# Kernel optimization log

Measured on AMD Instinct MI355X. Metric: run time of the kernel, lower is better.

Reference implementation:

```python
import jax, jax.numpy as jnp
import numpy as np

B, LAT, CIN, W, K, F = 16, 512, 512, 4096, 3, 512

def setup_inputs() -> dict:
    key = jax.random.key(0)
    k1, k2, k3, k4 = jax.random.split(key, 4)
    latent = jax.random.normal(k1, (B, LAT), jnp.float32)
    content = jax.random.normal(k2, (B, CIN, W), jnp.float32)
    # glorot_uniform for affine weight
    lim = np.sqrt(6.0 / (LAT + CIN))
    affine_w = jax.random.uniform(k3, (LAT, CIN), jnp.float32, -lim, lim)
    affine_b = jnp.zeros((1, CIN), jnp.float32)
    # he_normal for conv kernel (fan_in = K*CIN)
    kernel_w = jax.random.normal(k4, (K, CIN, F), jnp.float32) * np.sqrt(2.0 / (K * CIN))
    kernel_b = jnp.zeros((1, F, 1), jnp.float32)
    return {"latent": latent, "content": content, "affine_w": affine_w,
            "affine_b": affine_b, "kernel_w": kernel_w, "kernel_b": kernel_b}

def reference(latent, content, affine_w, affine_b, kernel_w, kernel_b):
    # style affine: [B, CIN]
    affine = latent @ affine_w + affine_b
    # demod scale per (b, f): 1/sqrt(sum_{k,c} (kernel[k,c,f]*affine[b,c])^2 + 1e-8)
    demod = jax.lax.rsqrt(jnp.einsum('kcf,bc->bf', kernel_w * kernel_w,
                                     affine * affine) + 1e-8)
    # modulate input instead of per-sample weights (mathematically identical,
    # avoids batch-as-groups grouped conv): x[b,c,w] = content * affine[b,c]
    x = content * affine[:, :, None]
    # shared-kernel conv1d, NCW / SAME; filter layout [K, CIN, F] == HIO
    y = jax.lax.conv_general_dilated(
        x, kernel_w, window_strides=(1,), padding='SAME',
        dimension_numbers=('NCH', 'HIO', 'NCH'))
    y = y * demod[:, :, None] + kernel_b  # [B, F, W]
    return jnp.where(y >= 0, y, 0.2 * y)  # leaky_relu(0.2)
```

## Files before the change

### kernel.cpp

```cpp
#include <hip/hip_runtime.h>
#include <hip/hip_bf16.h>

#define Bn   16
#define LATn 512
#define Cn   512
#define Wn   4096
#define Fn   512

using bf16x8 = __attribute__((ext_vector_type(8))) short;
using f32x4  = __attribute__((ext_vector_type(4))) float;

__device__ __forceinline__ unsigned short f2bf(float x) {
    union { float f; unsigned int u; } v; v.f = x;
    unsigned int r = v.u + 0x7fffu + ((v.u >> 16) & 1u);
    return (unsigned short)(r >> 16);
}

__device__ __forceinline__ void gload_lds16(const void* g, void* l) {
    __builtin_amdgcn_global_load_lds(
        (const __attribute__((address_space(1))) unsigned int*)g,
        (__attribute__((address_space(3))) unsigned int*)l, 16, 0, 0);
}

__global__ void k_affine(const float* __restrict__ latent,
                         const float* __restrict__ aw,
                         const float* __restrict__ ab,
                         float* __restrict__ affine,
                         float* __restrict__ zbuf) {
    if (blockIdx.x == 0 && blockIdx.y == 0 && threadIdx.x < 16)
        zbuf[threadIdx.x] = 0.f;
    __shared__ float red[4][64];
    const int t  = threadIdx.x;
    const int cl = t & 63, lq = t >> 6;
    const int c  = blockIdx.x * 64 + cl;
    const int b  = blockIdx.y;
    float s = 0.f;
    #pragma unroll 4
    for (int l = lq * 128; l < lq * 128 + 128; ++l)
        s = fmaf(latent[b * LATn + l], aw[(size_t)l * Cn + c], s);
    red[lq][cl] = s;
    __syncthreads();
    if (t < 64)
        affine[b * Cn + blockIdx.x * 64 + t] =
            red[0][t] + red[1][t] + red[2][t] + red[3][t] + ab[blockIdx.x * 64 + t];
}

__global__ void k_qsum(const float* __restrict__ kw, float* __restrict__ Q) {
    const int i = (blockIdx.x * 256 + threadIdx.x) * 4;
    const float4 a = *(const float4*)&kw[i];
    const float4 b = *(const float4*)&kw[Cn * Fn + i];
    const float4 c = *(const float4*)&kw[2 * Cn * Fn + i];
    float4 q;
    q.x = a.x * a.x + b.x * b.x + c.x * c.x;
    q.y = a.y * a.y + b.y * b.y + c.y * c.y;
    q.z = a.z * a.z + b.z * b.z + c.z * c.z;
    q.w = a.w * a.w + b.w * b.w + c.w * c.w;
    *(float4*)&Q[i] = q;
}

__global__ void k_demod2(const float* __restrict__ Q,
                         const float* __restrict__ affine,
                         float* __restrict__ demod) {
    __shared__ float red[4][64];
    const int t  = threadIdx.x;
    const int fl = t & 63, cq = t >> 6;
    const int f  = blockIdx.x * 64 + fl;
    const int b  = blockIdx.y;
    float s = 0.f;
    #pragma unroll 4
    for (int c = cq * 128; c < cq * 128 + 128; ++c) {
        const float a = affine[b * Cn + c];
        s = fmaf(a * a, Q[(size_t)c * Fn + f], s);
    }
    red[cq][fl] = s;
    __syncthreads();
    if (t < 64)
        demod[b * Fn + blockIdx.x * 64 + t] =
            rsqrtf(red[0][t] + red[1][t] + red[2][t] + red[3][t] + 1e-8f);
}

__global__ void k_tk(const float* __restrict__ kw, unsigned short* __restrict__ kt) {
    __shared__ float lds[32][65];
    const int t  = threadIdx.x;
    const int k  = blockIdx.z;
    const int c0 = blockIdx.x * 32;
    const int f0 = blockIdx.y * 64;
    #pragma unroll
    for (int i = 0; i < 8; ++i) {
        int e = t + 256 * i; int c = e >> 6; int f = e & 63;
        lds[c][f] = kw[((size_t)(k * Cn + c0 + c)) * Fn + f0 + f];
    }
    __syncthreads();
    #pragma unroll
    for (int i = 0; i < 8; ++i) {
        int e = t + 256 * i; int f = e >> 5; int c = e & 31;
        kt[((size_t)(k * Fn + f0 + f)) * Cn + c0 + c] = f2bf(lds[c][f]);
    }
}

__global__ void k_tx(const float* __restrict__ content,
                     const float* __restrict__ affine,
                     unsigned short* __restrict__ xt) {
    __shared__ unsigned short lds[64][72];
    const int t  = threadIdx.x;
    const int b  = blockIdx.z;
    const int c0 = blockIdx.y * 64;
    const int w0 = blockIdx.x * 64;
    #pragma unroll
    for (int i = 0; i < 4; ++i) {
        int e = t + 256 * i;
        int c = e >> 4;
        int w4 = (e & 15) * 4;
        float4 v = *(const float4*)&content[((size_t)(b * Cn + c0 + c)) * Wn + w0 + w4];
        float a = affine[b * Cn + c0 + c];
        int wx = w4 ^ ((c >> 3) << 3);
        unsigned short p[4] = {f2bf(v.x * a), f2bf(v.y * a), f2bf(v.z * a), f2bf(v.w * a)};
        *(uint2*)&lds[c][wx] = *(const uint2*)p;
    }
    __syncthreads();
    #pragma unroll
    for (int i = 0; i < 2; ++i) {
        int e = t + 256 * i;
        int w  = e >> 3;
        int q  = e & 7;
        int c8 = q * 8;
        int wx = w ^ (q << 3);
        unsigned short tmp[8];
        #pragma unroll
        for (int j = 0; j < 8; ++j) tmp[j] = lds[c8 + j][wx];
        *(uint4*)&xt[((size_t)b * Wn + w0 + w) * Cn + c0 + c8] = *(uint4*)tmp;
    }
}

#define BM 256
#define BN 256
#define BK 32
#define KBYTES (3 * BM * BK * 2)
#define BUFB   (KBYTES + BN * BK * 2)
#define SMEMB  (2 * BUFB + 2 * Cn * 2)

extern __shared__ __align__(16) char smem[];

#define ISSUE_XT(dst, c0s) { \
    _Pragma("unroll") for (int i_ = 0; i_ < 2; ++i_) { \
        const int Q_ = i_ * 512 + t; \
        const int r_ = Q_ >> 2; \
        const int j_ = (Q_ & 3) ^ ((r_ >> 1) & 3); \
        gload_lds16(&xt[((size_t)b * Wn + w0 + r_) * Cn + (c0s) + j_ * 8], \
                    (dst) + KBYTES + (size_t)Q_ * 16); } }

#define ISSUE_PLANE(dst, c0s, P) { \
    _Pragma("unroll") for (int i_ = 0; i_ < 2; ++i_) { \
        const int Q_ = i_ * 512 + t; \
        const int r_ = Q_ >> 2; \
        const int j_ = (Q_ & 3) ^ ((r_ >> 1) & 3); \
        gload_lds16(&kt[((size_t)((P) * Fn + f0 + r_)) * Cn + (c0s) + j_ * 8], \
                    (dst) + (size_t)((P) * 1024 + Q_) * 16); } }

#define PHASE(K, VM, ...) { \
    asm volatile("s_waitcnt vmcnt(" #VM ")" ::: "memory"); \
    asm volatile("s_barrier" ::: "memory"); \
    bf16x8 af[8]; bf16x8 bv[4]; \
    _Pragma("unroll") for (int m_ = 0; m_ < 8; ++m_) { \
        const int r_ = wm * 128 + m_ * 16 + l15; \
        af[m_] = *(const bf16x8*)(ka + ((K) * 256 + r_) * 32 + (lhi ^ ((r_ >> 1) & 3)) * 8); } \
    _Pragma("unroll") for (int n_ = 0; n_ < 4; ++n_) { \
        const int rl_ = wn * 64 + n_ * 16 + l15 + (K) - 1; \
        const unsigned short* bp_ = xa + rl_ * 32 + (lhi ^ ((rl_ >> 1) & 3)) * 8; \
        if ((K) == 0 && n_ == 0 && rl_ < 0)   bp_ = halo + c0 + lhi * 8; \
        if ((K) == 2 && n_ == 3 && rl_ > 255) bp_ = halo + 512 + c0 + lhi * 8; \
        bv[n_] = *(const bf16x8*)bp_; } \
    __VA_ARGS__; \
    asm volatile("s_waitcnt lgkmcnt(0)" ::: "memory"); \
    __builtin_amdgcn_sched_barrier(0); \
    __builtin_amdgcn_s_setprio(1); \
    _Pragma("unroll") for (int n_ = 0; n_ < 4; ++n_) \
        _Pragma("unroll") for (int m_ = 0; m_ < 8; ++m_) \
            acc[m_][n_] = __builtin_amdgcn_mfma_f32_16x16x32_bf16(af[m_], bv[n_], acc[m_][n_], 0, 0, 0); \
    __builtin_amdgcn_s_setprio(0); }

__global__ __launch_bounds__(512, 1)
void k_conv(const unsigned short* __restrict__ kt,
            const unsigned short* __restrict__ xt,
            const float* __restrict__ demod,
            const float* __restrict__ kb,
            const float* __restrict__ zbuf,
            float* __restrict__ y) {
    const int t  = threadIdx.x;
    const int w0 = blockIdx.x * BN;
    const int f0 = blockIdx.y * BM;
    const int b  = blockIdx.z;

    const int wave = t >> 6;
    const int lane = t & 63;
    const int wm   = wave >> 2;
    const int wn   = wave & 3;
    const int l15  = lane & 15;
    const int lhi  = lane >> 4;

    unsigned short* halo = (unsigned short*)(smem + 2 * BUFB);

    f32x4 acc[8][4];
    #pragma unroll
    for (int m = 0; m < 8; ++m)
        #pragma unroll
        for (int n = 0; n < 4; ++n)
            #pragma unroll
            for (int r = 0; r < 4; ++r)
                acc[m][n][r] = 0.f;

    if (t < 128) {
        const int h  = t >> 6;
        const int wg = h ? (w0 + BN) : (w0 - 1);
        const unsigned short* src = ((unsigned)wg < (unsigned)Wn)
            ? &xt[((size_t)b * Wn + wg) * Cn + (t & 63) * 8]
            : (const unsigned short*)zbuf;
        gload_lds16(src, halo + (size_t)t * 8);
    }
    ISSUE_XT(smem, 0);
    ISSUE_PLANE(smem, 0, 0);
    ISSUE_PLANE(smem, 0, 1);
    ISSUE_PLANE(smem, 0, 2);

    int cur = 0;
    for (int cc = 0; cc < Cn / BK; ++cc) {
        const unsigned short* ka = (const unsigned short*)(smem + cur * BUFB);
        const unsigned short* xa = ka + 3 * BM * BK;
        char* nbuf = smem + (cur ^ 1) * BUFB;
        const int c0 = cc * BK;
        const int c1 = c0 + BK;
        const bool pf = cc < Cn / BK - 1;
        PHASE(0, 4, if (pf) { ISSUE_XT(nbuf, c1); ISSUE_PLANE(nbuf, c1, 0); });
        PHASE(1, 6, if (pf) { ISSUE_PLANE(nbuf, c1, 1); });
        PHASE(2, 6, if (pf) { ISSUE_PLANE(nbuf, c1, 2); });
        cur ^= 1;
    }

    #pragma unroll
    for (int m = 0; m < 8; ++m) {
        const int fb = f0 + wm * 128 + m * 16 + lhi * 4;
        const float4 dmv = *(const float4*)&demod[b * Fn + fb];
        const float4 kbv = *(const float4*)&kb[fb];
        const float dmf[4] = {dmv.x, dmv.y, dmv.z, dmv.w};
        const float kbf[4] = {kbv.x, kbv.y, kbv.z, kbv.w};
        #pragma unroll
        for (int n = 0; n < 4; ++n) {
            const int w = w0 + wn * 64 + n * 16 + l15;
            #pragma unroll
            for (int r = 0; r < 4; ++r) {
                float v = fmaf(acc[m][n][r], dmf[r], kbf[r]);
                v = (v >= 0.f) ? v : 0.2f * v;
                y[((size_t)(b * Fn + fb + r)) * Wn + w] = v;
            }
        }
    }
}

extern "C" void kernel_launch(void* const* d_in, const int* in_sizes, int n_in,
                              void* d_out, int out_size, void* d_ws, size_t ws_size,
                              hipStream_t stream) {
    const float* latent  = (const float*)d_in[0];
    const float* content = (const float*)d_in[1];
    const float* aw      = (const float*)d_in[2];
    const float* ab      = (const float*)d_in[3];
    const float* kw      = (const float*)d_in[4];
    const float* kb      = (const float*)d_in[5];
    float* y = (float*)d_out;

    char* ws = (char*)d_ws;
    float*          affine = (float*)(ws);
    float*          demod  = (float*)(ws + 32768);
    float*          zbuf   = (float*)(ws + 65536);
    float*          Q      = (float*)(ws + 131072);
    unsigned short* kt     = (unsigned short*)(ws + 131072);
    unsigned short* xt     = (unsigned short*)(ws + 2u * 1024u * 1024u);
    if (ws_size < 2u * 1024u * 1024u + (size_t)Bn * Wn * Cn * 2u) return;

    hipFuncSetAttribute((const void*)k_conv,
                        hipFuncAttributeMaxDynamicSharedMemorySize, SMEMB);

    k_affine<<<dim3(Cn / 64, Bn),           256, 0, stream>>>(latent, aw, ab, affine, zbuf);
    k_qsum  <<<dim3(Cn * Fn / 1024),        256, 0, stream>>>(kw, Q);
    k_demod2<<<dim3(Fn / 64, Bn),           256, 0, stream>>>(Q, affine, demod);
    k_tk    <<<dim3(Cn / 32, Fn / 64, 3),   256, 0, stream>>>(kw, kt);
    k_tx    <<<dim3(Wn / 64, Cn / 64, Bn),  256, 0, stream>>>(content, affine, xt);
    k_conv  <<<dim3(Wn / BN, Fn / BM, Bn),  512, SMEMB, stream>>>(kt, xt, demod, kb, zbuf, y);
}
```

Before: 167.1 us.

## Split conv phases into half-M sub-phases with ping-pong barriers

Each K-plane phase is split into two halves over the M tiles, so each wave loads only 4 A fragments at a time and reuses the B fragments across both halves. The next-chunk prefetch is spread across the sub-phases. Synchronisation changes from per-phase vmcnt waits to a full vmcnt(0) wait at the end of each chunk, with a barrier before and after every MFMA block. This aims to lower register pressure and interleave LDS reads with MFMA work, but it adds barriers and makes the global-load wait coarser.

```diff
diff --git a/kernel.cpp b/kernel.cpp
--- a/kernel.cpp
+++ b/kernel.cpp
@@ -157,27 +157,31 @@
         gload_lds16(&kt[((size_t)((P) * Fn + f0 + r_)) * Cn + (c0s) + j_ * 8], \
                     (dst) + (size_t)((P) * 1024 + Q_) * 16); } }
 
-#define PHASE(K, VM, ...) { \
-    asm volatile("s_waitcnt vmcnt(" #VM ")" ::: "memory"); \
+#define PHASE(K, H, PRE, POSTW) { \
+    if ((H) == 0) { \
+        _Pragma("unroll") for (int n_ = 0; n_ < 4; ++n_) { \
+            const int rl_ = wn * 64 + n_ * 16 + l15 + (K) - 1; \
+            const unsigned short* bp_ = xa + rl_ * 32 + (lhi ^ ((rl_ >> 1) & 3)) * 8; \
+            if ((K) == 0 && n_ == 0 && rl_ < 0)   bp_ = halo + c0 + lhi * 8; \
+            if ((K) == 2 && n_ == 3 && rl_ > 255) bp_ = halo + 512 + c0 + lhi * 8; \
+            bv[n_] = *(const bf16x8*)bp_; } \
+    } \
+    bf16x8 af[4]; \
+    _Pragma("unroll") for (int m_ = 0; m_ < 4; ++m_) { \
+        const int r_ = wm * 128 + ((H) * 4 + m_) * 16 + l15; \
+        af[m_] = *(const bf16x8*)(ka + ((K) * 256 + r_) * 32 + (lhi ^ ((r_ >> 1) & 3)) * 8); } \
+    PRE; \
     asm volatile("s_barrier" ::: "memory"); \
-    bf16x8 af[8]; bf16x8 bv[4]; \
-    _Pragma("unroll") for (int m_ = 0; m_ < 8; ++m_) { \
-        const int r_ = wm * 128 + m_ * 16 + l15; \
-        af[m_] = *(const bf16x8*)(ka + ((K) * 256 + r_) * 32 + (lhi ^ ((r_ >> 1) & 3)) * 8); } \
-    _Pragma("unroll") for (int n_ = 0; n_ < 4; ++n_) { \
-        const int rl_ = wn * 64 + n_ * 16 + l15 + (K) - 1; \
-        const unsigned short* bp_ = xa + rl_ * 32 + (lhi ^ ((rl_ >> 1) & 3)) * 8; \
-        if ((K) == 0 && n_ == 0 && rl_ < 0)   bp_ = halo + c0 + lhi * 8; \
-        if ((K) == 2 && n_ == 3 && rl_ > 255) bp_ = halo + 512 + c0 + lhi * 8; \
-        bv[n_] = *(const bf16x8*)bp_; } \
-    __VA_ARGS__; \
     asm volatile("s_waitcnt lgkmcnt(0)" ::: "memory"); \
     __builtin_amdgcn_sched_barrier(0); \
     __builtin_amdgcn_s_setprio(1); \
     _Pragma("unroll") for (int n_ = 0; n_ < 4; ++n_) \
-        _Pragma("unroll") for (int m_ = 0; m_ < 8; ++m_) \
-            acc[m_][n_] = __builtin_amdgcn_mfma_f32_16x16x32_bf16(af[m_], bv[n_], acc[m_][n_], 0, 0, 0); \
-    __builtin_amdgcn_s_setprio(0); }
+        _Pragma("unroll") for (int m_ = 0; m_ < 4; ++m_) \
+            acc[(H) * 4 + m_][n_] = __builtin_amdgcn_mfma_f32_16x16x32_bf16( \
+                af[m_], bv[n_], acc[(H) * 4 + m_][n_], 0, 0, 0); \
+    __builtin_amdgcn_s_setprio(0); \
+    POSTW; \
+    asm volatile("s_barrier" ::: "memory"); }
 
 __global__ __launch_bounds__(512, 1)
 void k_conv(const unsigned short* __restrict__ kt,
@@ -221,6 +225,8 @@
     ISSUE_PLANE(smem, 0, 0);
     ISSUE_PLANE(smem, 0, 1);
     ISSUE_PLANE(smem, 0, 2);
+    asm volatile("s_waitcnt vmcnt(0)" ::: "memory");
+    asm volatile("s_barrier" ::: "memory");
 
     int cur = 0;
     for (int cc = 0; cc < Cn / BK; ++cc) {
@@ -230,9 +236,13 @@
         const int c0 = cc * BK;
         const int c1 = c0 + BK;
         const bool pf = cc < Cn / BK - 1;
-        PHASE(0, 4, if (pf) { ISSUE_XT(nbuf, c1); ISSUE_PLANE(nbuf, c1, 0); });
-        PHASE(1, 6, if (pf) { ISSUE_PLANE(nbuf, c1, 1); });
-        PHASE(2, 6, if (pf) { ISSUE_PLANE(nbuf, c1, 2); });
+        bf16x8 bv[4];
+        PHASE(0, 0, if (pf) { ISSUE_XT(nbuf, c1); },      )
+        PHASE(0, 1, if (pf) { ISSUE_PLANE(nbuf, c1, 0); },)
+        PHASE(1, 0, if (pf) { ISSUE_PLANE(nbuf, c1, 1); },)
+        PHASE(1, 1, if (pf) { ISSUE_PLANE(nbuf, c1, 2); },)
+        PHASE(2, 0, ,                                     )
+        PHASE(2, 1, , asm volatile("s_waitcnt vmcnt(0)" ::: "memory"))
         cur ^= 1;
     }
 
```

Result: slower. 170.5 us (+2.1%).

## Switch conv GEMM to 32x32 MFMA, merge prep kernels, load halo rows directly

Applied to the files above, without the earlier changes.

The conv main loop now uses 32x32x16 bf16 MFMA tiles in place of 16x16x32, which gives fewer instructions and fewer LDS fragment reads for each output. The activation tile is loaded as 258 rows so the halo sits in the same buffer, and a small zeroed LDS slot replaces the global zero buffer. The q-sum, demod, kernel-transpose and content-transpose kernels are merged into one launch, and the last iteration is peeled so the loop carries no prefetch branch. This cuts launch count and LDS traffic, at the cost of more registers per MFMA tile and more complex halo and waitcnt bookkeeping.

```diff
diff --git a/kernel.cpp b/kernel.cpp
--- a/kernel.cpp
+++ b/kernel.cpp
@@ -8,7 +8,7 @@
 #define Fn   512
 
 using bf16x8 = __attribute__((ext_vector_type(8))) short;
-using f32x4  = __attribute__((ext_vector_type(4))) float;
+using f32x16 = __attribute__((ext_vector_type(16))) float;
 
 __device__ __forceinline__ unsigned short f2bf(float x) {
     union { float f; unsigned int u; } v; v.f = x;
@@ -25,10 +25,7 @@
 __global__ void k_affine(const float* __restrict__ latent,
                          const float* __restrict__ aw,
                          const float* __restrict__ ab,
-                         float* __restrict__ affine,
-                         float* __restrict__ zbuf) {
-    if (blockIdx.x == 0 && blockIdx.y == 0 && threadIdx.x < 16)
-        zbuf[threadIdx.x] = 0.f;
+                         float* __restrict__ affine) {
     __shared__ float red[4][64];
     const int t  = threadIdx.x;
     const int cl = t & 63, lq = t >> 6;
@@ -45,99 +42,95 @@
             red[0][t] + red[1][t] + red[2][t] + red[3][t] + ab[blockIdx.x * 64 + t];
 }
 
-__global__ void k_qsum(const float* __restrict__ kw, float* __restrict__ Q) {
-    const int i = (blockIdx.x * 256 + threadIdx.x) * 4;
-    const float4 a = *(const float4*)&kw[i];
-    const float4 b = *(const float4*)&kw[Cn * Fn + i];
-    const float4 c = *(const float4*)&kw[2 * Cn * Fn + i];
-    float4 q;
-    q.x = a.x * a.x + b.x * b.x + c.x * c.x;
-    q.y = a.y * a.y + b.y * b.y + c.y * c.y;
-    q.z = a.z * a.z + b.z * b.z + c.z * c.z;
-    q.w = a.w * a.w + b.w * b.w + c.w * c.w;
-    *(float4*)&Q[i] = q;
-}
-
-__global__ void k_demod2(const float* __restrict__ Q,
-                         const float* __restrict__ affine,
-                         float* __restrict__ demod) {
-    __shared__ float red[4][64];
-    const int t  = threadIdx.x;
-    const int fl = t & 63, cq = t >> 6;
-    const int f  = blockIdx.x * 64 + fl;
-    const int b  = blockIdx.y;
-    float s = 0.f;
-    #pragma unroll 4
-    for (int c = cq * 128; c < cq * 128 + 128; ++c) {
-        const float a = affine[b * Cn + c];
-        s = fmaf(a * a, Q[(size_t)c * Fn + f], s);
-    }
-    red[cq][fl] = s;
-    __syncthreads();
-    if (t < 64)
-        demod[b * Fn + blockIdx.x * 64 + t] =
-            rsqrtf(red[0][t] + red[1][t] + red[2][t] + red[3][t] + 1e-8f);
-}
-
-__global__ void k_tk(const float* __restrict__ kw, unsigned short* __restrict__ kt) {
-    __shared__ float lds[32][65];
-    const int t  = threadIdx.x;
-    const int k  = blockIdx.z;
-    const int c0 = blockIdx.x * 32;
-    const int f0 = blockIdx.y * 64;
-    #pragma unroll
-    for (int i = 0; i < 8; ++i) {
-        int e = t + 256 * i; int c = e >> 6; int f = e & 63;
-        lds[c][f] = kw[((size_t)(k * Cn + c0 + c)) * Fn + f0 + f];
-    }
-    __syncthreads();
-    #pragma unroll
-    for (int i = 0; i < 8; ++i) {
-        int e = t + 256 * i; int f = e >> 5; int c = e & 31;
-        kt[((size_t)(k * Fn + f0 + f)) * Cn + c0 + c] = f2bf(lds[c][f]);
-    }
-}
-
-__global__ void k_tx(const float* __restrict__ content,
-                     const float* __restrict__ affine,
-                     unsigned short* __restrict__ xt) {
-    __shared__ unsigned short lds[64][72];
-    const int t  = threadIdx.x;
-    const int b  = blockIdx.z;
-    const int c0 = blockIdx.y * 64;
-    const int w0 = blockIdx.x * 64;
-    #pragma unroll
-    for (int i = 0; i < 4; ++i) {
-        int e = t + 256 * i;
-        int c = e >> 4;
-        int w4 = (e & 15) * 4;
-        float4 v = *(const float4*)&content[((size_t)(b * Cn + c0 + c)) * Wn + w0 + w4];
-        float a = affine[b * Cn + c0 + c];
-        int wx = w4 ^ ((c >> 3) << 3);
-        unsigned short p[4] = {f2bf(v.x * a), f2bf(v.y * a), f2bf(v.z * a), f2bf(v.w * a)};
-        *(uint2*)&lds[c][wx] = *(const uint2*)p;
-    }
-    __syncthreads();
-    #pragma unroll
-    for (int i = 0; i < 2; ++i) {
-        int e = t + 256 * i;
-        int w  = e >> 3;
-        int q  = e & 7;
-        int c8 = q * 8;
-        int wx = w ^ (q << 3);
-        unsigned short tmp[8];
-        #pragma unroll
-        for (int j = 0; j < 8; ++j) tmp[j] = lds[c8 + j][wx];
-        *(uint4*)&xt[((size_t)b * Wn + w0 + w) * Cn + c0 + c8] = *(uint4*)tmp;
+__global__ __launch_bounds__(256)
+void k_mid(const float* __restrict__ kw,
+           const float* __restrict__ affine,
+           const float* __restrict__ content,
+           float* __restrict__ demod,
+           unsigned short* __restrict__ kt,
+           unsigned short* __restrict__ xt) {
+    __shared__ __align__(16) char shraw[9216];
+    const int t   = threadIdx.x;
+    const int bid = blockIdx.x;
+
+    if (bid < 128) {
+        float (*red)[64] = (float(*)[64])shraw;
+        const int fl = t & 63, cq = t >> 6;
+        const int f  = (bid & 7) * 64 + fl;
+        const int b  = bid >> 3;
+        float s = 0.f;
+        for (int c = cq * 128; c < cq * 128 + 128; ++c) {
+            const float a  = affine[b * Cn + c];
+            const float k0 = kw[((size_t)(0 * Cn + c)) * Fn + f];
+            const float k1 = kw[((size_t)(1 * Cn + c)) * Fn + f];
+            const float k2 = kw[((size_t)(2 * Cn + c)) * Fn + f];
+            s = fmaf(k0 * k0 + k1 * k1 + k2 * k2, a * a, s);
+        }
+        red[cq][fl] = s;
+        __syncthreads();
+        if (t < 64)
+            demod[b * Fn + (bid & 7) * 64 + t] =
+                rsqrtf(red[0][t] + red[1][t] + red[2][t] + red[3][t] + 1e-8f);
+    } else if (bid < 512) {
+        float (*lds)[65] = (float(*)[65])shraw;
+        const int e  = bid - 128;
+        const int k  = e / 128;
+        const int e2 = e % 128;
+        const int c0 = (e2 & 15) * 32;
+        const int f0 = (e2 >> 4) * 64;
+        #pragma unroll
+        for (int i = 0; i < 8; ++i) {
+            int q = t + 256 * i; int c = q >> 6; int f = q & 63;
+            lds[c][f] = kw[((size_t)(k * Cn + c0 + c)) * Fn + f0 + f];
+        }
+        __syncthreads();
+        #pragma unroll
+        for (int i = 0; i < 8; ++i) {
+            int q = t + 256 * i; int f = q >> 5; int c = q & 31;
+            kt[((size_t)(k * Fn + f0 + f)) * Cn + c0 + c] = f2bf(lds[c][f]);
+        }
+    } else {
+        unsigned short (*lds)[72] = (unsigned short(*)[72])shraw;
+        const int e  = bid - 512;
+        const int w0 = (e & 63) * 64;
+        const int c0 = ((e >> 6) & 7) * 64;
+        const int b  = e >> 9;
+        #pragma unroll
+        for (int i = 0; i < 4; ++i) {
+            int q = t + 256 * i;
+            int c = q >> 4;
+            int w4 = (q & 15) * 4;
+            float4 v = *(const float4*)&content[((size_t)(b * Cn + c0 + c)) * Wn + w0 + w4];
+            float a = affine[b * Cn + c0 + c];
+            int wx = w4 ^ ((c >> 3) << 3);
+            unsigned short p[4] = {f2bf(v.x * a), f2bf(v.y * a), f2bf(v.z * a), f2bf(v.w * a)};
+            *(uint2*)&lds[c][wx] = *(const uint2*)p;
+        }
+        __syncthreads();
+        #pragma unroll
+        for (int i = 0; i < 2; ++i) {
+            int q  = t + 256 * i;
+            int w  = q >> 3;
+            int qq = q & 7;
+            int c8 = qq * 8;
+            int wx = w ^ (qq << 3);
+            unsigned short tmp[8];
+            #pragma unroll
+            for (int j = 0; j < 8; ++j) tmp[j] = lds[c8 + j][wx];
+            *(uint4*)&xt[((size_t)b * Wn + w0 + w) * Cn + c0 + c8] = *(uint4*)tmp;
+        }
     }
 }
 
 #define BM 256
 #define BN 256
 #define BK 32
-#define KBYTES (3 * BM * BK * 2)
-#define BUFB   (KBYTES + BN * BK * 2)
-#define SMEMB  (2 * BUFB + 2 * Cn * 2)
+#define ABYTES (3 * BM * BK * 2)
+#define XROWS  258
+#define XBYTES (XROWS * BK * 2)
+#define BUFB   (ABYTES + XBYTES)
+#define ZOFF   (2 * BUFB)
+#define SMEMB  (ZOFF + 64)
 
 extern __shared__ __align__(16) char smem[];
 
@@ -146,13 +139,21 @@
         const int Q_ = i_ * 512 + t; \
         const int r_ = Q_ >> 2; \
         const int j_ = (Q_ & 3) ^ ((r_ >> 1) & 3); \
-        gload_lds16(&xt[((size_t)b * Wn + w0 + r_) * Cn + (c0s) + j_ * 8], \
-                    (dst) + KBYTES + (size_t)Q_ * 16); } }
+        int wg_ = w0 - 1 + r_; wg_ = wg_ < 0 ? 0 : wg_; \
+        gload_lds16(&xt[((size_t)b * Wn + wg_) * Cn + (c0s) + j_ * 8], \
+                    (dst) + ABYTES + (size_t)Q_ * 16); } \
+    { const int Q_ = 1024 + wave; \
+      const int r_ = Q_ >> 2; \
+      const int j_ = (Q_ & 3) ^ ((r_ >> 1) & 3); \
+      int wg_ = w0 - 1 + r_; wg_ = wg_ > Wn - 1 ? Wn - 1 : wg_; \
+      if (lane == 0) \
+          gload_lds16(&xt[((size_t)b * Wn + wg_) * Cn + (c0s) + j_ * 8], \
+                      (dst) + ABYTES + (size_t)Q_ * 16); } }
 
 #define ISSUE_PLANE(dst, c0s, P) { \
     _Pragma("unroll") for (int i_ = 0; i_ < 2; ++i_) { \
         const int Q_ = i_ * 512 + t; \
-        const int r_ = Q_ >> 2; \
+        const int r_ = (Q_ >> 2) & 255; \
         const int j_ = (Q_ & 3) ^ ((r_ >> 1) & 3); \
         gload_lds16(&kt[((size_t)((P) * Fn + f0 + r_)) * Cn + (c0s) + j_ * 8], \
                     (dst) + (size_t)((P) * 1024 + Q_) * 16); } }
@@ -161,22 +162,28 @@
     asm volatile("s_waitcnt vmcnt(" #VM ")" ::: "memory"); \
     asm volatile("s_barrier" ::: "memory"); \
     bf16x8 af[8]; bf16x8 bv[4]; \
-    _Pragma("unroll") for (int m_ = 0; m_ < 8; ++m_) { \
-        const int r_ = wm * 128 + m_ * 16 + l15; \
-        af[m_] = *(const bf16x8*)(ka + ((K) * 256 + r_) * 32 + (lhi ^ ((r_ >> 1) & 3)) * 8); } \
-    _Pragma("unroll") for (int n_ = 0; n_ < 4; ++n_) { \
-        const int rl_ = wn * 64 + n_ * 16 + l15 + (K) - 1; \
-        const unsigned short* bp_ = xa + rl_ * 32 + (lhi ^ ((rl_ >> 1) & 3)) * 8; \
-        if ((K) == 0 && n_ == 0 && rl_ < 0)   bp_ = halo + c0 + lhi * 8; \
-        if ((K) == 2 && n_ == 3 && rl_ > 255) bp_ = halo + 512 + c0 + lhi * 8; \
-        bv[n_] = *(const bf16x8*)bp_; } \
+    _Pragma("unroll") for (int mt_ = 0; mt_ < 4; ++mt_) \
+    _Pragma("unroll") for (int ks_ = 0; ks_ < 2; ++ks_) { \
+        const int r_ = wm * 128 + mt_ * 32 + l31; \
+        af[mt_ * 2 + ks_] = *(const bf16x8*)(ka + ((K) * 256 + r_) * 32 \
+            + ((ks_ * 2 + lhi2) ^ ((r_ >> 1) & 3)) * 8); } \
+    _Pragma("unroll") for (int nt_ = 0; nt_ < 2; ++nt_) \
+    _Pragma("unroll") for (int ks_ = 0; ks_ < 2; ++ks_) { \
+        const int gw_ = w0 + wn * 64 + nt_ * 32 + l31 + (K) - 1; \
+        const int rw_ = wn * 64 + nt_ * 32 + l31 + (K);           \
+        const unsigned short* bp_ = xa + rw_ * 32 + ((ks_ * 2 + lhi2) ^ ((rw_ >> 1) & 3)) * 8; \
+        if ((K) == 0 && nt_ == 0) bp_ = (gw_ < 0)      ? zl : bp_; \
+        if ((K) == 2 && nt_ == 1) bp_ = (gw_ > Wn - 1) ? zl : bp_; \
+        bv[nt_ * 2 + ks_] = *(const bf16x8*)bp_; } \
     __VA_ARGS__; \
     asm volatile("s_waitcnt lgkmcnt(0)" ::: "memory"); \
     __builtin_amdgcn_sched_barrier(0); \
     __builtin_amdgcn_s_setprio(1); \
-    _Pragma("unroll") for (int n_ = 0; n_ < 4; ++n_) \
-        _Pragma("unroll") for (int m_ = 0; m_ < 8; ++m_) \
-            acc[m_][n_] = __builtin_amdgcn_mfma_f32_16x16x32_bf16(af[m_], bv[n_], acc[m_][n_], 0, 0, 0); \
+    _Pragma("unroll") for (int ks_ = 0; ks_ < 2; ++ks_) \
+    _Pragma("unroll") for (int nt_ = 0; nt_ < 2; ++nt_) \
+    _Pragma("unroll") for (int mt_ = 0; mt_ < 4; ++mt_) \
+        acc[mt_][nt_] = __builtin_amdgcn_mfma_f32_32x32x16_bf16( \
+            af[mt_ * 2 + ks_], bv[nt_ * 2 + ks_], acc[mt_][nt_], 0, 0, 0); \
     __builtin_amdgcn_s_setprio(0); }
 
 __global__ __launch_bounds__(512, 1)
@@ -184,7 +191,6 @@
             const unsigned short* __restrict__ xt,
             const float* __restrict__ demod,
             const float* __restrict__ kb,
-            const float* __restrict__ zbuf,
             float* __restrict__ y) {
     const int t  = threadIdx.x;
     const int w0 = blockIdx.x * BN;
@@ -195,62 +201,64 @@
     const int lane = t & 63;
     const int wm   = wave >> 2;
     const int wn   = wave & 3;
-    const int l15  = lane & 15;
-    const int lhi  = lane >> 4;
-
-    unsigned short* halo = (unsigned short*)(smem + 2 * BUFB);
-
-    f32x4 acc[8][4];
+    const int l31  = lane & 31;
+    const int lhi2 = lane >> 5;
+
+    const unsigned short* zl = (const unsigned short*)(smem + ZOFF);
+
+    f32x16 acc[4][2];
     #pragma unroll
-    for (int m = 0; m < 8; ++m)
-        #pragma unroll
-        for (int n = 0; n < 4; ++n)
+    for (int m = 0; m < 4; ++m)
+        #pragma unroll
+        for (int n = 0; n < 2; ++n)
             #pragma unroll
-            for (int r = 0; r < 4; ++r)
+            for (int r = 0; r < 16; ++r)
                 acc[m][n][r] = 0.f;
 
-    if (t < 128) {
-        const int h  = t >> 6;
-        const int wg = h ? (w0 + BN) : (w0 - 1);
-        const unsigned short* src = ((unsigned)wg < (unsigned)Wn)
-            ? &xt[((size_t)b * Wn + wg) * Cn + (t & 63) * 8]
-            : (const unsigned short*)zbuf;
-        gload_lds16(src, halo + (size_t)t * 8);
-    }
+    if (t < 4) { uint4 z = {0u, 0u, 0u, 0u}; *(uint4*)(smem + ZOFF + t * 16) = z; }
     ISSUE_XT(smem, 0);
     ISSUE_PLANE(smem, 0, 0);
     ISSUE_PLANE(smem, 0, 1);
     ISSUE_PLANE(smem, 0, 2);
+    asm volatile("s_waitcnt lgkmcnt(0)" ::: "memory");
 
     int cur = 0;
-    for (int cc = 0; cc < Cn / BK; ++cc) {
+    for (int cc = 0; cc < Cn / BK - 1; ++cc) {
         const unsigned short* ka = (const unsigned short*)(smem + cur * BUFB);
         const unsigned short* xa = ka + 3 * BM * BK;
         char* nbuf = smem + (cur ^ 1) * BUFB;
-        const int c0 = cc * BK;
-        const int c1 = c0 + BK;
-        const bool pf = cc < Cn / BK - 1;
-        PHASE(0, 4, if (pf) { ISSUE_XT(nbuf, c1); ISSUE_PLANE(nbuf, c1, 0); });
-        PHASE(1, 6, if (pf) { ISSUE_PLANE(nbuf, c1, 1); });
-        PHASE(2, 6, if (pf) { ISSUE_PLANE(nbuf, c1, 2); });
+        const int c1 = (cc + 1) * BK;
+        PHASE(0, 4, ISSUE_XT(nbuf, c1); ISSUE_PLANE(nbuf, c1, 0);)
+        PHASE(1, 7, ISSUE_PLANE(nbuf, c1, 1);)
+        PHASE(2, 7, ISSUE_PLANE(nbuf, c1, 2);)
         cur ^= 1;
     }
+    {
+        const unsigned short* ka = (const unsigned short*)(smem + cur * BUFB);
+        const unsigned short* xa = ka + 3 * BM * BK;
+        PHASE(0, 4, )
+        PHASE(1, 2, )
+        PHASE(2, 0, )
+    }
 
     #pragma unroll
-    for (int m = 0; m < 8; ++m) {
-        const int fb = f0 + wm * 128 + m * 16 + lhi * 4;
-        const float4 dmv = *(const float4*)&demod[b * Fn + fb];
-        const float4 kbv = *(const float4*)&kb[fb];
-        const float dmf[4] = {dmv.x, dmv.y, dmv.z, dmv.w};
-        const float kbf[4] = {kbv.x, kbv.y, kbv.z, kbv.w};
-        #pragma unroll
-        for (int n = 0; n < 4; ++n) {
-            const int w = w0 + wn * 64 + n * 16 + l15;
+    for (int mt = 0; mt < 4; ++mt) {
+        #pragma unroll
+        for (int g = 0; g < 4; ++g) {
+            const int fb = f0 + wm * 128 + mt * 32 + g * 8 + lhi2 * 4;
+            const float4 dm = *(const float4*)&demod[b * Fn + fb];
+            const float4 kv = *(const float4*)&kb[fb];
+            const float dmf[4] = {dm.x, dm.y, dm.z, dm.w};
+            const float kbf[4] = {kv.x, kv.y, kv.z, kv.w};
             #pragma unroll
-            for (int r = 0; r < 4; ++r) {
-                float v = fmaf(acc[m][n][r], dmf[r], kbf[r]);
-                v = (v >= 0.f) ? v : 0.2f * v;
-                y[((size_t)(b * Fn + fb + r)) * Wn + w] = v;
+            for (int nt = 0; nt < 2; ++nt) {
+                const int w = w0 + wn * 64 + nt * 32 + l31;
+                #pragma unroll
+                for (int r2 = 0; r2 < 4; ++r2) {
+                    float v = fmaf(acc[mt][nt][g * 4 + r2], dmf[r2], kbf[r2]);
+                    v = (v >= 0.f) ? v : 0.2f * v;
+                    y[((size_t)(b * Fn + fb + r2)) * Wn + w] = v;
+                }
             }
         }
     }
@@ -270,8 +278,6 @@
     char* ws = (char*)d_ws;
     float*          affine = (float*)(ws);
     float*          demod  = (float*)(ws + 32768);
-    float*          zbuf   = (float*)(ws + 65536);
-    float*          Q      = (float*)(ws + 131072);
     unsigned short* kt     = (unsigned short*)(ws + 131072);
     unsigned short* xt     = (unsigned short*)(ws + 2u * 1024u * 1024u);
     if (ws_size < 2u * 1024u * 1024u + (size_t)Bn * Wn * Cn * 2u) return;
@@ -279,10 +285,8 @@
     hipFuncSetAttribute((const void*)k_conv,
                         hipFuncAttributeMaxDynamicSharedMemorySize, SMEMB);
 
-    k_affine<<<dim3(Cn / 64, Bn),           256, 0, stream>>>(latent, aw, ab, affine, zbuf);
-    k_qsum  <<<dim3(Cn * Fn / 1024),        256, 0, stream>>>(kw, Q);
-    k_demod2<<<dim3(Fn / 64, Bn),           256, 0, stream>>>(Q, affine, demod);
-    k_tk    <<<dim3(Cn / 32, Fn / 64, 3),   256, 0, stream>>>(kw, kt);
-    k_tx    <<<dim3(Wn / 64, Cn / 64, Bn),  256, 0, stream>>>(content, affine, xt);
-    k_conv  <<<dim3(Wn / BN, Fn / BM, Bn),  512, SMEMB, stream>>>(kt, xt, demod, kb, zbuf, y);
-}
+    k_affine<<<dim3(Cn / 64, Bn),          256, 0, stream>>>(latent, aw, ab, affine);
+    k_mid   <<<dim3(128 + 384 + Wn / 64 * Cn / 64 * Bn), 256, 0, stream>>>(
+            kw, affine, content, demod, kt, xt);
+    k_conv  <<<dim3(Wn / BN, Fn / BM, Bn), 512, SMEMB, stream>>>(kt, xt, demod, kb, y);
+}
```

After: 165.9 us. No clear change (-0.7%).

## Merge demod, kernel transpose and input transpose into one launch; peel last conv iteration

Applied to the files above, without the earlier changes.

Fuses the qsum, demod, weight-transpose and input-modulate/transpose kernels into a single block-indexed kernel, and computes the squared-weight sum inline so the Q buffer is gone. This removes three kernel launches, their inter-kernel gaps and one intermediate write/read. The conv main loop now peels its final K-chunk so the prefetch predicate leaves the steady-state loop and the tail uses tighter waitcnts. The plane-issue row index is also masked to 255. The cost is that demod blocks re-read kw with strided loads, and the fused kernel's branches give its blocks uneven work.

```diff
diff --git a/kernel.cpp b/kernel.cpp
--- a/kernel.cpp
+++ b/kernel.cpp
@@ -45,90 +45,83 @@
             red[0][t] + red[1][t] + red[2][t] + red[3][t] + ab[blockIdx.x * 64 + t];
 }
 
-__global__ void k_qsum(const float* __restrict__ kw, float* __restrict__ Q) {
-    const int i = (blockIdx.x * 256 + threadIdx.x) * 4;
-    const float4 a = *(const float4*)&kw[i];
-    const float4 b = *(const float4*)&kw[Cn * Fn + i];
-    const float4 c = *(const float4*)&kw[2 * Cn * Fn + i];
-    float4 q;
-    q.x = a.x * a.x + b.x * b.x + c.x * c.x;
-    q.y = a.y * a.y + b.y * b.y + c.y * c.y;
-    q.z = a.z * a.z + b.z * b.z + c.z * c.z;
-    q.w = a.w * a.w + b.w * b.w + c.w * c.w;
-    *(float4*)&Q[i] = q;
-}
-
-__global__ void k_demod2(const float* __restrict__ Q,
-                         const float* __restrict__ affine,
-                         float* __restrict__ demod) {
-    __shared__ float red[4][64];
-    const int t  = threadIdx.x;
-    const int fl = t & 63, cq = t >> 6;
-    const int f  = blockIdx.x * 64 + fl;
-    const int b  = blockIdx.y;
-    float s = 0.f;
-    #pragma unroll 4
-    for (int c = cq * 128; c < cq * 128 + 128; ++c) {
-        const float a = affine[b * Cn + c];
-        s = fmaf(a * a, Q[(size_t)c * Fn + f], s);
-    }
-    red[cq][fl] = s;
-    __syncthreads();
-    if (t < 64)
-        demod[b * Fn + blockIdx.x * 64 + t] =
-            rsqrtf(red[0][t] + red[1][t] + red[2][t] + red[3][t] + 1e-8f);
-}
-
-__global__ void k_tk(const float* __restrict__ kw, unsigned short* __restrict__ kt) {
-    __shared__ float lds[32][65];
-    const int t  = threadIdx.x;
-    const int k  = blockIdx.z;
-    const int c0 = blockIdx.x * 32;
-    const int f0 = blockIdx.y * 64;
-    #pragma unroll
-    for (int i = 0; i < 8; ++i) {
-        int e = t + 256 * i; int c = e >> 6; int f = e & 63;
-        lds[c][f] = kw[((size_t)(k * Cn + c0 + c)) * Fn + f0 + f];
-    }
-    __syncthreads();
-    #pragma unroll
-    for (int i = 0; i < 8; ++i) {
-        int e = t + 256 * i; int f = e >> 5; int c = e & 31;
-        kt[((size_t)(k * Fn + f0 + f)) * Cn + c0 + c] = f2bf(lds[c][f]);
-    }
-}
-
-__global__ void k_tx(const float* __restrict__ content,
-                     const float* __restrict__ affine,
-                     unsigned short* __restrict__ xt) {
-    __shared__ unsigned short lds[64][72];
-    const int t  = threadIdx.x;
-    const int b  = blockIdx.z;
-    const int c0 = blockIdx.y * 64;
-    const int w0 = blockIdx.x * 64;
-    #pragma unroll
-    for (int i = 0; i < 4; ++i) {
-        int e = t + 256 * i;
-        int c = e >> 4;
-        int w4 = (e & 15) * 4;
-        float4 v = *(const float4*)&content[((size_t)(b * Cn + c0 + c)) * Wn + w0 + w4];
-        float a = affine[b * Cn + c0 + c];
-        int wx = w4 ^ ((c >> 3) << 3);
-        unsigned short p[4] = {f2bf(v.x * a), f2bf(v.y * a), f2bf(v.z * a), f2bf(v.w * a)};
-        *(uint2*)&lds[c][wx] = *(const uint2*)p;
-    }
-    __syncthreads();
-    #pragma unroll
-    for (int i = 0; i < 2; ++i) {
-        int e = t + 256 * i;
-        int w  = e >> 3;
-        int q  = e & 7;
-        int c8 = q * 8;
-        int wx = w ^ (q << 3);
-        unsigned short tmp[8];
-        #pragma unroll
-        for (int j = 0; j < 8; ++j) tmp[j] = lds[c8 + j][wx];
-        *(uint4*)&xt[((size_t)b * Wn + w0 + w) * Cn + c0 + c8] = *(uint4*)tmp;
+__global__ __launch_bounds__(256)
+void k_mid(const float* __restrict__ kw,
+           const float* __restrict__ affine,
+           const float* __restrict__ content,
+           float* __restrict__ demod,
+           unsigned short* __restrict__ kt,
+           unsigned short* __restrict__ xt) {
+    __shared__ __align__(16) char shraw[9216];
+    const int t   = threadIdx.x;
+    const int bid = blockIdx.x;
+
+    if (bid < 128) {
+        float (*red)[64] = (float(*)[64])shraw;
+        const int fl = t & 63, cq = t >> 6;
+        const int f  = (bid & 7) * 64 + fl;
+        const int b  = bid >> 3;
+        float s = 0.f;
+        for (int c = cq * 128; c < cq * 128 + 128; ++c) {
+            const float a  = affine[b * Cn + c];
+            const float k0 = kw[((size_t)(0 * Cn + c)) * Fn + f];
+            const float k1 = kw[((size_t)(1 * Cn + c)) * Fn + f];
+            const float k2 = kw[((size_t)(2 * Cn + c)) * Fn + f];
+            s = fmaf(k0 * k0 + k1 * k1 + k2 * k2, a * a, s);
+        }
+        red[cq][fl] = s;
+        __syncthreads();
+        if (t < 64)
+            demod[b * Fn + (bid & 7) * 64 + t] =
+                rsqrtf(red[0][t] + red[1][t] + red[2][t] + red[3][t] + 1e-8f);
+    } else if (bid < 512) {
+        float (*lds)[65] = (float(*)[65])shraw;
+        const int e  = bid - 128;
+        const int k  = e / 128;
+        const int e2 = e % 128;
+        const int c0 = (e2 & 15) * 32;
+        const int f0 = (e2 >> 4) * 64;
+        #pragma unroll
+        for (int i = 0; i < 8; ++i) {
+            int q = t + 256 * i; int c = q >> 6; int f = q & 63;
+            lds[c][f] = kw[((size_t)(k * Cn + c0 + c)) * Fn + f0 + f];
+        }
+        __syncthreads();
+        #pragma unroll
+        for (int i = 0; i < 8; ++i) {
+            int q = t + 256 * i; int f = q >> 5; int c = q & 31;
+            kt[((size_t)(k * Fn + f0 + f)) * Cn + c0 + c] = f2bf(lds[c][f]);
+        }
+    } else {
+        unsigned short (*lds)[72] = (unsigned short(*)[72])shraw;
+        const int e  = bid - 512;
+        const int w0 = (e & 63) * 64;
+        const int c0 = ((e >> 6) & 7) * 64;
+        const int b  = e >> 9;
+        #pragma unroll
+        for (int i = 0; i < 4; ++i) {
+            int q = t + 256 * i;
+            int c = q >> 4;
+            int w4 = (q & 15) * 4;
+            float4 v = *(const float4*)&content[((size_t)(b * Cn + c0 + c)) * Wn + w0 + w4];
+            float a = affine[b * Cn + c0 + c];
+            int wx = w4 ^ ((c >> 3) << 3);
+            unsigned short p[4] = {f2bf(v.x * a), f2bf(v.y * a), f2bf(v.z * a), f2bf(v.w * a)};
+            *(uint2*)&lds[c][wx] = *(const uint2*)p;
+        }
+        __syncthreads();
+        #pragma unroll
+        for (int i = 0; i < 2; ++i) {
+            int q  = t + 256 * i;
+            int w  = q >> 3;
+            int qq = q & 7;
+            int c8 = qq * 8;
+            int wx = w ^ (qq << 3);
+            unsigned short tmp[8];
+            #pragma unroll
+            for (int j = 0; j < 8; ++j) tmp[j] = lds[c8 + j][wx];
+            *(uint4*)&xt[((size_t)b * Wn + w0 + w) * Cn + c0 + c8] = *(uint4*)tmp;
+        }
     }
 }
 
@@ -152,7 +145,7 @@
 #define ISSUE_PLANE(dst, c0s, P) { \
     _Pragma("unroll") for (int i_ = 0; i_ < 2; ++i_) { \
         const int Q_ = i_ * 512 + t; \
-        const int r_ = Q_ >> 2; \
+        const int r_ = (Q_ >> 2) & 255; \
         const int j_ = (Q_ & 3) ^ ((r_ >> 1) & 3); \
         gload_lds16(&kt[((size_t)((P) * Fn + f0 + r_)) * Cn + (c0s) + j_ * 8], \
                     (dst) + (size_t)((P) * 1024 + Q_) * 16); } }
@@ -223,17 +216,24 @@
     ISSUE_PLANE(smem, 0, 2);
 
     int cur = 0;
-    for (int cc = 0; cc < Cn / BK; ++cc) {
+    for (int cc = 0; cc < Cn / BK - 1; ++cc) {
         const unsigned short* ka = (const unsigned short*)(smem + cur * BUFB);
         const unsigned short* xa = ka + 3 * BM * BK;
         char* nbuf = smem + (cur ^ 1) * BUFB;
         const int c0 = cc * BK;
         const int c1 = c0 + BK;
-        const bool pf = cc < Cn / BK - 1;
-        PHASE(0, 4, if (pf) { ISSUE_XT(nbuf, c1); ISSUE_PLANE(nbuf, c1, 0); });
-        PHASE(1, 6, if (pf) { ISSUE_PLANE(nbuf, c1, 1); });
-        PHASE(2, 6, if (pf) { ISSUE_PLANE(nbuf, c1, 2); });
+        PHASE(0, 4, ISSUE_XT(nbuf, c1); ISSUE_PLANE(nbuf, c1, 0);)
+        PHASE(1, 6, ISSUE_PLANE(nbuf, c1, 1);)
+        PHASE(2, 6, ISSUE_PLANE(nbuf, c1, 2);)
         cur ^= 1;
+    }
+    {
+        const unsigned short* ka = (const unsigned short*)(smem + cur * BUFB);
+        const unsigned short* xa = ka + 3 * BM * BK;
+        const int c0 = Cn - BK;
+        PHASE(0, 4, )
+        PHASE(1, 2, )
+        PHASE(2, 0, )
     }
 
     #pragma unroll
@@ -271,7 +271,6 @@
     float*          affine = (float*)(ws);
     float*          demod  = (float*)(ws + 32768);
     float*          zbuf   = (float*)(ws + 65536);
-    float*          Q      = (float*)(ws + 131072);
     unsigned short* kt     = (unsigned short*)(ws + 131072);
     unsigned short* xt     = (unsigned short*)(ws + 2u * 1024u * 1024u);
     if (ws_size < 2u * 1024u * 1024u + (size_t)Bn * Wn * Cn * 2u) return;
@@ -279,10 +278,7 @@
     hipFuncSetAttribute((const void*)k_conv,
                         hipFuncAttributeMaxDynamicSharedMemorySize, SMEMB);
 
-    k_affine<<<dim3(Cn / 64, Bn),           256, 0, stream>>>(latent, aw, ab, affine, zbuf);
-    k_qsum  <<<dim3(Cn * Fn / 1024),        256, 0, stream>>>(kw, Q);
-    k_demod2<<<dim3(Fn / 64, Bn),           256, 0, stream>>>(Q, affine, demod);
-    k_tk    <<<dim3(Cn / 32, Fn / 64, 3),   256, 0, stream>>>(kw, kt);
-    k_tx    <<<dim3(Wn / 64, Cn / 64, Bn),  256, 0, stream>>>(content, affine, xt);
-    k_conv  <<<dim3(Wn / BN, Fn / BM, Bn),  512, SMEMB, stream>>>(kt, xt, demod, kb, zbuf, y);
-}
+    k_affine<<<dim3(Cn / 64, Bn),                        256, 0, stream>>>(latent, aw, ab, affine, zbuf);
+    k_mid   <<<dim3(128 + 384 + Wn / 64 * Cn / 64 * Bn), 256, 0, stream>>>(kw, affine, content, demod, kt, xt);
+    k_conv  <<<dim3(Wn / BN, Fn / BM, Bn),               512, SMEMB, stream>>>(kt, xt, demod, kb, zbuf, y);
+}
```

New measurement: 154.4 us. 7.6% less time.
